# Optimization experiments

Hardware: AMD Instinct MI355X
Metric: run time of the kernel (lower is better)

Reference implementation:

```python
import jax, jax.numpy as jnp
import numpy as np

N, E, G = 10000, 160000, 64
F, C1, C2, C3, K, NC = 128, 128, 256, 512, 5, 10


def setup_inputs() -> dict:
    key = jax.random.key(0)
    ks = jax.random.split(key, 12)
    s = 0.05
    return {
        "x": jax.random.normal(ks[0], (N, F), dtype=jnp.float32),
        "edge_index": jax.random.randint(ks[1], (2, E), 0, N, dtype=jnp.int64),
        "batch": jnp.sort(jax.random.randint(ks[2], (N,), 0, G, dtype=jnp.int64)),
        "W_cheb": jax.random.normal(ks[3], (K, F, C1), dtype=jnp.float32) * s,
        "b_cheb": jnp.zeros((C1,), jnp.float32),
        "W_g1": jax.random.normal(ks[4], (C1, C2), dtype=jnp.float32) * s,
        "b_g1": jnp.zeros((C2,), jnp.float32),
        "W_g2": jax.random.normal(ks[5], (C2, C3), dtype=jnp.float32) * s,
        "b_g2": jnp.zeros((C3,), jnp.float32),
        "w_gate": jax.random.normal(ks[6], (C3, 1), dtype=jnp.float32) * s,
        "b_gate": jnp.zeros((1,), jnp.float32),
        "W_fc": jax.random.normal(ks[7], (C3, NC), dtype=jnp.float32) * s,
        "b_fc": jnp.zeros((NC,), jnp.float32),
    }


def _deg_inv_sqrt(deg):
    return jnp.where(deg > 0, jax.lax.rsqrt(jnp.maximum(deg, 1e-12)), 0.0)


def cheb_conv(x, src, dst, W, b):
    # PyG ChebConv, sym normalization, lambda_max=2 => scaled Laplacian = -D^-1/2 A D^-1/2
    ones = jnp.ones((src.shape[0],), x.dtype)
    deg = jax.ops.segment_sum(ones, src, num_segments=N)
    dinv = _deg_inv_sqrt(deg)
    w = -(dinv[src] * dinv[dst])  # [E]

    def prop(h):
        return jax.ops.segment_sum(w[:, None] * h[src], dst, num_segments=N)

    tx0 = x
    tx1 = prop(x)
    out = tx0 @ W[0] + tx1 @ W[1]
    for k in range(2, W.shape[0]):
        tx2 = 2.0 * prop(tx1) - tx0
        out = out + tx2 @ W[k]
        tx0, tx1 = tx1, tx2
    return out + b


def gcn_conv(x, src, dst, W, b):
    # PyG GCNConv: add self-loops, sym norm D~^-1/2 (A+I) D~^-1/2, transform then aggregate
    loop = jnp.arange(N, dtype=src.dtype)
    src_a = jnp.concatenate([src, loop])
    dst_a = jnp.concatenate([dst, loop])
    ones = jnp.ones((src_a.shape[0],), x.dtype)
    deg = jax.ops.segment_sum(ones, dst_a, num_segments=N)
    dinv = _deg_inv_sqrt(deg)
    norm = dinv[src_a] * dinv[dst_a]  # [E+N]
    h = x @ W
    return jax.ops.segment_sum(norm[:, None] * h[src_a], dst_a, num_segments=N) + b


def attention_pool(x, batch, w_gate, b_gate):
    logits = (x @ w_gate + b_gate)[:, 0]  # [N]
    m = jax.ops.segment_max(logits, batch, num_segments=G)
    e = jnp.exp(logits - m[batch])
    s = jax.ops.segment_sum(e, batch, num_segments=G)
    alpha = e / s[batch]
    return jax.ops.segment_sum(alpha[:, None] * x, batch, num_segments=G)  # [G, C3]


def reference(x, edge_index, batch, W_cheb, b_cheb, W_g1, b_g1, W_g2, b_g2,
              w_gate, b_gate, W_fc, b_fc):
    src, dst = edge_index[0], edge_index[1]
    h = jax.nn.relu(cheb_conv(x, src, dst, W_cheb, b_cheb))
    h = jax.nn.relu(gcn_conv(h, src, dst, W_g1, b_g1))
    h = jax.nn.relu(gcn_conv(h, src, dst, W_g2, b_g2))
    g = attention_pool(h, batch, w_gate, b_gate)
    logits = g @ W_fc + b_fc
    return jax.nn.log_softmax(logits, axis=1)
```

## Files before the change

kernel.cpp:

```cpp
#include <hip/hip_runtime.h>
#include <hip/hip_bf16.h>
#include <math.h>

#define N_NODES 10000
#define N_EDGES 160000
#define N_GRAPHS 64
#define F_IN    128
#define C1_DIM  128
#define C2_DIM  256
#define C3_DIM  512
#define K_CHEB  5
#define NCLS    10
#define TC      (K_CHEB * F_IN)

typedef short v8s __attribute__((ext_vector_type(8)));
typedef float v4f __attribute__((ext_vector_type(4)));

static __device__ __forceinline__ unsigned short f2bf(float f) {
    unsigned u = __float_as_uint(f);
    unsigned r = (u + 0x7FFFu + ((u >> 16) & 1u)) >> 16;
    return (unsigned short)r;
}
static __device__ __forceinline__ float bf_lo(unsigned u) { return __uint_as_float(u << 16); }
static __device__ __forceinline__ float bf_hi(unsigned u) { return __uint_as_float(u & 0xFFFF0000u); }

#define PREP_A (N_NODES * 32)
#define PREP_B (TC * C1_DIM)
#define PREP_C (C1_DIM * C2_DIM)
#define PREP_D (C2_DIM * C3_DIM)
#define PREP_E N_NODES
#define PREP_F N_NODES
#define PREP_G N_EDGES
#define PREP_TOTAL (PREP_A + PREP_B + PREP_C + PREP_D + PREP_E + PREP_F + PREP_G)
__global__ void prep_kernel(const float* __restrict__ x, unsigned short* __restrict__ tcat,
                            const float* __restrict__ Wcheb, unsigned short* __restrict__ Wcb_t,
                            const float* __restrict__ Wg1, unsigned short* __restrict__ Wg1_t,
                            const float* __restrict__ Wg2, unsigned short* __restrict__ Wg2_t,
                            const int* __restrict__ batch, int* __restrict__ gptr,
                            float* __restrict__ logits,
                            const int* __restrict__ src, const int* __restrict__ dst,
                            int* __restrict__ cnt_s, int* __restrict__ cnt_d) {
    int id = blockIdx.x * blockDim.x + threadIdx.x;
    if (id < PREP_A) {
        int n = id >> 5, f = (id & 31) * 4;
        float4 v = *(const float4*)(x + (size_t)n * F_IN + f);
        ushort4 o; o.x = f2bf(v.x); o.y = f2bf(v.y); o.z = f2bf(v.z); o.w = f2bf(v.w);
        *(ushort4*)(tcat + (size_t)n * TC + f) = o;
        return;
    }
    id -= PREP_A;
    if (id < PREP_B) {
        int k = id % TC, n = id / TC;
        Wcb_t[(size_t)n * TC + k] = f2bf(Wcheb[(size_t)k * C1_DIM + n]);
        return;
    }
    id -= PREP_B;
    if (id < PREP_C) {
        int k = id % C1_DIM, n = id / C1_DIM;
        Wg1_t[(size_t)n * C1_DIM + k] = f2bf(Wg1[(size_t)k * C2_DIM + n]);
        return;
    }
    id -= PREP_C;
    if (id < PREP_D) {
        int k = id % C2_DIM, n = id / C2_DIM;
        Wg2_t[(size_t)n * C2_DIM + k] = f2bf(Wg2[(size_t)k * C3_DIM + n]);
        return;
    }
    id -= PREP_D;
    if (id < PREP_E) {
        int i = id;
        int b = batch[i];
        if (i == 0) { for (int g = 0; g <= b; g++) gptr[g] = 0; }
        else {
            int bp = batch[i - 1];
            for (int g = bp + 1; g <= b; g++) gptr[g] = i;
        }
        if (i == N_NODES - 1) { for (int g = b + 1; g <= N_GRAPHS; g++) gptr[g] = N_NODES; }
        return;
    }
    id -= PREP_E;
    if (id < PREP_F) { logits[id] = 0.0f; return; }
    id -= PREP_F;
    if (id < PREP_G) {
        atomicAdd(&cnt_s[src[id]], 1);
        atomicAdd(&cnt_d[dst[id]], 1);
    }
}

__global__ __launch_bounds__(256) void fill_scan_kernel(
        const int* __restrict__ src, const int* __restrict__ dst,
        const int* __restrict__ cnt_s, const int* __restrict__ cnt_d,
        int* __restrict__ rowptr, int* __restrict__ fillc,
        int2* __restrict__ ecb, int2* __restrict__ egc, int E, int n) {
    __shared__ int ldsc[N_NODES];
    __shared__ int sums[256];
    int tid = threadIdx.x;
    for (int i = tid; i < n; i += 256) ldsc[i] = cnt_d[i];
    __syncthreads();
    int chunk = (n + 255) / 256;
    int s0 = min(n, tid * chunk), s1 = min(n, s0 + chunk);
    int loc = 0;
    for (int i = s0; i < s1; i++) loc += ldsc[i];
    sums[tid] = loc;
    __syncthreads();
    for (int off = 1; off < 256; off <<= 1) {
        int t = (tid >= off) ? sums[tid - off] : 0;
        __syncthreads();
        sums[tid] += t;
        __syncthreads();
    }
    int pre = sums[tid] - loc;
    for (int i = s0; i < s1; i++) { int v = ldsc[i]; ldsc[i] = pre; pre += v; }
    __syncthreads();
    if (blockIdx.x == 0) {
        for (int i = tid; i < n; i += 256) rowptr[i] = ldsc[i];
        if (tid == 255) rowptr[n] = pre;
    }
    int e = blockIdx.x * 256 + tid;
    if (e >= E) return;
    int s = src[e], d = dst[e];
    int pos = ldsc[d] + atomicAdd(&fillc[d], 1);
    int cs = cnt_s[s], cd = cnt_s[d];
    float ds = (cs > 0) ? rsqrtf((float)cs) : 0.0f;
    float dd = (cd > 0) ? rsqrtf((float)cd) : 0.0f;
    float nr = rsqrtf((float)cnt_d[s] + 1.0f) * rsqrtf((float)cnt_d[d] + 1.0f);
    ecb[pos] = make_int2(s, __float_as_int(-(ds * dd)));
    egc[pos] = make_int2(s, __float_as_int(nr));
}

__global__ __launch_bounds__(256) void gather_cheb_bf(
        const unsigned short* __restrict__ tb, const int* __restrict__ rowptr,
        const int2* __restrict__ edges,
        const unsigned short* __restrict__ base, float alpha, float beta,
        unsigned short* __restrict__ outc, int n) {
    int w = (blockIdx.x * blockDim.x + threadIdx.x) >> 6;
    int lane = threadIdx.x & 63;
    if (w >= n) return;
    w = __builtin_amdgcn_readfirstlane(w);
    int rs = __builtin_amdgcn_readfirstlane(rowptr[w]);
    int re = __builtin_amdgcn_readfirstlane(rowptr[w + 1]);
    float a0 = 0.0f, a1 = 0.0f;
    for (int b = rs; b < re; b += 64) {
        int nv = min(64, re - b);
        int cl = 0, wlb = 0;
        if (b + lane < re) { int2 e = edges[b + lane]; cl = e.x; wlb = e.y; }
        int nk = (nv + 15) & ~15;
        for (int j = 0; j < nk; j += 16) {
            int ss[16]; float ww[16]; unsigned uu[16];
            #pragma unroll
            for (int q = 0; q < 16; q++) {
                ss[q] = __builtin_amdgcn_readlane(cl, j + q);
                ww[q] = __uint_as_float((unsigned)__builtin_amdgcn_readlane(wlb, j + q));
            }
            #pragma unroll
            for (int q = 0; q < 16; q++)
                uu[q] = *(const unsigned*)(tb + (size_t)ss[q] * TC + lane * 2);
            #pragma unroll
            for (int q = 0; q < 16; q++) { a0 += ww[q] * bf_lo(uu[q]); a1 += ww[q] * bf_hi(uu[q]); }
        }
    }
    if (base) {
        unsigned ub = ((const unsigned*)(base + (size_t)w * TC))[lane];
        a0 = alpha * a0 + beta * bf_lo(ub);
        a1 = alpha * a1 + beta * bf_hi(ub);
    } else {
        a0 *= alpha; a1 *= alpha;
    }
    ushort2 o; o.x = f2bf(a0); o.y = f2bf(a1);
    *(ushort2*)(outc + (size_t)w * TC + lane * 2) = o;
}

template<int FPL>
__global__ __launch_bounds__(256) void gather_gcn_pre(
        const unsigned short* __restrict__ tb, const int* __restrict__ rowptr,
        const int2* __restrict__ edges,
        const int* __restrict__ cnt_d, unsigned short* __restrict__ z, int n) {
    const int C = FPL * 64;
    int w = (blockIdx.x * blockDim.x + threadIdx.x) >> 6;
    int lane = threadIdx.x & 63;
    if (w >= n) return;
    w = __builtin_amdgcn_readfirstlane(w);
    int rs = __builtin_amdgcn_readfirstlane(rowptr[w]);
    int re = __builtin_amdgcn_readfirstlane(rowptr[w + 1]);
    float acc[FPL];
    #pragma unroll
    for (int q = 0; q < FPL; q++) acc[q] = 0.0f;
    for (int b = rs; b < re; b += 64) {
        int nv = min(64, re - b);
        int cl = 0, wlb = 0;
        if (b + lane < re) { int2 e = edges[b + lane]; cl = e.x; wlb = e.y; }
        int nk = (nv + 15) & ~15;
        for (int j = 0; j < nk; j += 16) {
            int ss[16]; float ww[16];
            #pragma unroll
            for (int q = 0; q < 16; q++) {
                ss[q] = __builtin_amdgcn_readlane(cl, j + q);
                ww[q] = __uint_as_float((unsigned)__builtin_amdgcn_readlane(wlb, j + q));
            }
            if constexpr (FPL == 2) {
                unsigned uu[16];
                #pragma unroll
                for (int q = 0; q < 16; q++)
                    uu[q] = *(const unsigned*)(tb + (size_t)ss[q] * C + lane * 2);
                #pragma unroll
                for (int q = 0; q < 16; q++) { acc[0] += ww[q] * bf_lo(uu[q]); acc[1] += ww[q] * bf_hi(uu[q]); }
            } else {
                uint2 uu[16];
                #pragma unroll
                for (int q = 0; q < 16; q++)
                    uu[q] = *(const uint2*)(tb + (size_t)ss[q] * C + lane * 4);
                #pragma unroll
                for (int q = 0; q < 16; q++) {
                    acc[0] += ww[q] * bf_lo(uu[q].x); acc[1] += ww[q] * bf_hi(uu[q].x);
                    acc[2] += ww[q] * bf_lo(uu[q].y); acc[3] += ww[q] * bf_hi(uu[q].y);
                }
            }
        }
    }
    float sn = 1.0f / (float)(cnt_d[w] + 1);
    if constexpr (FPL == 2) {
        unsigned u = ((const unsigned*)(tb + (size_t)w * C))[lane];
        acc[0] += sn * bf_lo(u); acc[1] += sn * bf_hi(u);
        ushort2 o; o.x = f2bf(acc[0]); o.y = f2bf(acc[1]);
        *(ushort2*)(z + (size_t)w * C + lane * 2) = o;
    } else {
        uint2 u = ((const uint2*)(tb + (size_t)w * C))[lane];
        acc[0] += sn * bf_lo(u.x); acc[1] += sn * bf_hi(u.x);
        acc[2] += sn * bf_lo(u.y); acc[3] += sn * bf_hi(u.y);
        ushort4 o; o.x = f2bf(acc[0]); o.y = f2bf(acc[1]);
        o.z = f2bf(acc[2]); o.w = f2bf(acc[3]);
        *(ushort4*)(z + (size_t)w * C + lane * 4) = o;
    }
}

template<int JT, int KC>
__global__ __launch_bounds__(256) void gemm_bf16(
        const unsigned short* __restrict__ A, const unsigned short* __restrict__ Bt,
        const float* __restrict__ bias,
        unsigned short* __restrict__ Cb, const float* __restrict__ wg,
        float* __restrict__ logits, int M, int N) {
    int m0 = blockIdx.y * 64, n0 = blockIdx.x * (JT * 32);
    int wave = threadIdx.x >> 6, lane = threadIdx.x & 63;
    int wm = (wave & 1) * 32, wn = (wave >> 1) * (JT * 16);
    int l15 = lane & 15, quad = lane >> 4;

    v4f acc[2][JT];
    #pragma unroll
    for (int i = 0; i < 2; i++)
        #pragma unroll
        for (int j = 0; j < JT; j++) acc[i][j] = (v4f){0.f, 0.f, 0.f, 0.f};

    const unsigned short* Ab[2]; bool av[2];
    #pragma unroll
    for (int i = 0; i < 2; i++) {
        int row = m0 + wm + i * 16 + l15;
        av[i] = row < M;
        Ab[i] = A + (size_t)(av[i] ? row : 0) * KC + quad * 8;
    }
    const unsigned short* Bb[JT];
    #pragma unroll
    for (int j = 0; j < JT; j++) {
        int coln = n0 + wn + j * 16 + l15;
        Bb[j] = Bt + (size_t)coln * KC + quad * 8;
    }
    const v8s zero8 = {0, 0, 0, 0, 0, 0, 0, 0};

    #pragma unroll
    for (int k0 = 0; k0 < KC; k0 += 32) {
        v8s a[2], b[JT];
        #pragma unroll
        for (int i = 0; i < 2; i++) a[i] = av[i] ? *(const v8s*)(Ab[i] + k0) : zero8;
        #pragma unroll
        for (int j = 0; j < JT; j++) b[j] = *(const v8s*)(Bb[j] + k0);
        #pragma unroll
        for (int i = 0; i < 2; i++)
            #pragma unroll
            for (int j = 0; j < JT; j++)
                acc[i][j] = __builtin_amdgcn_mfma_f32_16x16x32_bf16(a[i], b[j], acc[i][j], 0, 0, 0);
    }

    float bv[JT], wgj[JT];
    #pragma unroll
    for (int j = 0; j < JT; j++) {
        int coln = n0 + wn + j * 16 + l15;
        bv[j] = bias[coln];
        wgj[j] = wg ? wg[coln] : 0.0f;
    }
    #pragma unroll
    for (int i = 0; i < 2; i++) {
        #pragma unroll
        for (int r = 0; r < 4; r++) {
            int row = m0 + wm + i * 16 + quad * 4 + r;
            if (row >= M) continue;
            float gval = 0.0f;
            #pragma unroll
            for (int j = 0; j < JT; j++) {
                int coln = n0 + wn + j * 16 + l15;
                float v = fmaxf(acc[i][j][r] + bv[j], 0.0f);
                Cb[(size_t)row * N + coln] = f2bf(v);
                gval += v * wgj[j];
            }
            if (wg) {
                #pragma unroll
                for (int off = 1; off < 16; off <<= 1) gval += __shfl_xor(gval, off);
                if (l15 == 0) atomicAdd(&logits[row], gval);
            }
        }
    }
}

__global__ __launch_bounds__(256) void pool_fc_kernel(
        const unsigned short* __restrict__ h3b,
        const float* __restrict__ logits, const int* __restrict__ gptr,
        const float* __restrict__ Wfc, const float* __restrict__ bfc,
        float* __restrict__ out) {
    __shared__ float red[256];
    __shared__ float pl[C3_DIM];
    int g = blockIdx.x, tid = threadIdx.x;
    int gs = gptr[g], ge = gptr[g + 1];
    float m = -INFINITY;
    for (int i = gs + tid; i < ge; i += 256) m = fmaxf(m, logits[i]);
    red[tid] = m; __syncthreads();
    for (int off = 128; off > 0; off >>= 1) {
        if (tid < off) red[tid] = fmaxf(red[tid], red[tid + off]);
        __syncthreads();
    }
    m = red[0]; __syncthreads();
    float s = 0.0f;
    for (int i = gs + tid; i < ge; i += 256) s += expf(logits[i] - m);
    red[tid] = s; __syncthreads();
    for (int off = 128; off > 0; off >>= 1) {
        if (tid < off) red[tid] += red[tid + off];
        __syncthreads();
    }
    s = red[0];
    float sinv = (s > 0.0f) ? 1.0f / s : 0.0f;
    float a0 = 0.0f, a1 = 0.0f;
    for (int i = gs; i < ge; i++) {
        float al = expf(logits[i] - m) * sinv;
        unsigned u = ((const unsigned*)(h3b + (size_t)i * C3_DIM))[tid];
        a0 += al * bf_lo(u);
        a1 += al * bf_hi(u);
    }
    pl[tid * 2 + 0] = a0;
    pl[tid * 2 + 1] = a1;
    __syncthreads();
    if (tid < 64) {
        float acc = -INFINITY;
        if (tid < NCLS) {
            acc = bfc[tid];
            for (int k = 0; k < C3_DIM; k++)
                acc += pl[k] * Wfc[k * NCLS + tid];
        }
        float mm = acc;
        #pragma unroll
        for (int off = 8; off > 0; off >>= 1) mm = fmaxf(mm, __shfl_xor(mm, off, 16));
        float e = (tid < NCLS) ? expf(acc - mm) : 0.0f;
        float ss = e;
        #pragma unroll
        for (int off = 8; off > 0; off >>= 1) ss += __shfl_xor(ss, off, 16);
        if (tid < NCLS) out[g * NCLS + tid] = acc - mm - logf(ss);
    }
}

extern "C" void kernel_launch(void* const* d_in, const int* in_sizes, int n_in,
                              void* d_out, int out_size, void* d_ws, size_t ws_size,
                              hipStream_t stream) {
    const float* x      = (const float*)d_in[0];
    const int*   ei     = (const int*)d_in[1];
    const int*   batch  = (const int*)d_in[2];
    const float* W_cheb = (const float*)d_in[3];
    const float* b_cheb = (const float*)d_in[4];
    const float* W_g1   = (const float*)d_in[5];
    const float* b_g1   = (const float*)d_in[6];
    const float* W_g2   = (const float*)d_in[7];
    const float* b_g2   = (const float*)d_in[8];
    const float* w_gate = (const float*)d_in[9];
    const float* W_fc   = (const float*)d_in[11];
    const float* b_fc   = (const float*)d_in[12];
    const int* src = ei;
    const int* dst = ei + N_EDGES;
    float* out = (float*)d_out;

    const int N = N_NODES, E = N_EDGES, G = N_GRAPHS;

    char* Wp = (char*)d_ws;
    auto alloc = [&](size_t bytes) {
        void* p = Wp;
        Wp += (bytes + 255) & ~(size_t)255;
        return p;
    };
    int*   cnt3    = (int*)alloc((size_t)3 * N * 4);
    int*   cnt_s   = cnt3;
    int*   cnt_d   = cnt3 + N;
    int*   fillc   = cnt3 + 2 * N;
    int*   rowptr  = (int*)alloc((N + 1) * 4);
    int2*  ecb     = (int2*)alloc((size_t)E * 8);
    int2*  egc     = (int2*)alloc((size_t)E * 8);
    unsigned short* tcat  = (unsigned short*)alloc((size_t)N * TC * 2);
    unsigned short* h1b   = (unsigned short*)alloc((size_t)N * C1_DIM * 2);
    unsigned short* z1b   = (unsigned short*)alloc((size_t)N * C1_DIM * 2);
    unsigned short* h2b   = (unsigned short*)alloc((size_t)N * C2_DIM * 2);
    unsigned short* z2b   = (unsigned short*)alloc((size_t)N * C2_DIM * 2);
    unsigned short* h3b   = (unsigned short*)alloc((size_t)N * C3_DIM * 2);
    unsigned short* Wcb_t = (unsigned short*)alloc((size_t)TC * C1_DIM * 2);
    unsigned short* Wg1_t = (unsigned short*)alloc((size_t)C1_DIM * C2_DIM * 2);
    unsigned short* Wg2_t = (unsigned short*)alloc((size_t)C2_DIM * C3_DIM * 2);
    float* logits  = (float*)alloc(N * 4);
    int*   gptr    = (int*)alloc((G + 1) * 4);

    dim3 blk(256);
    auto cdiv = [](int a, int b) { return (a + b - 1) / b; };

    hipMemsetAsync(cnt3, 0, (size_t)3 * N * sizeof(int), stream);
    hipLaunchKernelGGL(prep_kernel, dim3(cdiv(PREP_TOTAL, 256)), blk, 0, stream,
                       x, tcat, W_cheb, Wcb_t, W_g1, Wg1_t, W_g2, Wg2_t,
                       batch, gptr, logits, src, dst, cnt_s, cnt_d);

    hipLaunchKernelGGL(fill_scan_kernel, dim3(cdiv(E, 256)), blk, 0, stream,
                       src, dst, cnt_s, cnt_d, rowptr, fillc, ecb, egc, E, N);

    const int NWB = cdiv(N, 4);

    hipLaunchKernelGGL(gather_cheb_bf, dim3(NWB), blk, 0, stream,
                       tcat + 0 * F_IN, rowptr, ecb,
                       (const unsigned short*)nullptr, 1.0f, 0.0f, tcat + 1 * F_IN, N);
    hipLaunchKernelGGL(gather_cheb_bf, dim3(NWB), blk, 0, stream,
                       tcat + 1 * F_IN, rowptr, ecb,
                       tcat + 0 * F_IN, 2.0f, -1.0f, tcat + 2 * F_IN, N);
    hipLaunchKernelGGL(gather_cheb_bf, dim3(NWB), blk, 0, stream,
                       tcat + 2 * F_IN, rowptr, ecb,
                       tcat + 1 * F_IN, 2.0f, -1.0f, tcat + 3 * F_IN, N);
    hipLaunchKernelGGL(gather_cheb_bf, dim3(NWB), blk, 0, stream,
                       tcat + 3 * F_IN, rowptr, ecb,
                       tcat + 2 * F_IN, 2.0f, -1.0f, tcat + 4 * F_IN, N);

    hipLaunchKernelGGL((gemm_bf16<2, TC>), dim3(C1_DIM / 64, cdiv(N, 64)), blk, 0, stream,
                       tcat, Wcb_t, b_cheb, h1b,
                       (const float*)nullptr, (float*)nullptr, N, C1_DIM);

    hipLaunchKernelGGL(gather_gcn_pre<2>, dim3(NWB), blk, 0, stream,
                       h1b, rowptr, egc, cnt_d, z1b, N);
    hipLaunchKernelGGL((gemm_bf16<4, C1_DIM>), dim3(C2_DIM / 128, cdiv(N, 64)), blk, 0, stream,
                       z1b, Wg1_t, b_g1, h2b,
                       (const float*)nullptr, (float*)nullptr, N, C2_DIM);

    hipLaunchKernelGGL(gather_gcn_pre<4>, dim3(NWB), blk, 0, stream,
                       h2b, rowptr, egc, cnt_d, z2b, N);
    hipLaunchKernelGGL((gemm_bf16<4, C2_DIM>), dim3(C3_DIM / 128, cdiv(N, 64)), blk, 0, stream,
                       z2b, Wg2_t, b_g2, h3b,
                       w_gate, logits, N, C3_DIM);

    hipLaunchKernelGGL(pool_fc_kernel, dim3(G), blk, 0, stream,
                       h3b, logits, gptr, W_fc, b_fc, out);
}
```

Before: 290.5 us.

## Fuse GCN gather into GEMM via LDS tile and split attention pooling across blocks

Each GCN layer's neighbor aggregation is now computed straight into a swizzled LDS tile inside the GEMM kernel, which removes the separate gather kernels and the z1/z2 intermediate buffers and their global round trips. The aggregation is recomputed once per column block: twice for layer 1 and twice for layer 2, which uses a wider JT=8 tile. Pooling is split into 8 node slices per graph that accumulate with float atomics, and the last block to finish does the FC and log-softmax. The cost is redundant gather work, larger LDS use that may lower occupancy, and non-deterministic atomic summation order.

```diff
diff --git a/kernel.cpp b/kernel.cpp
--- a/kernel.cpp
+++ b/kernel.cpp
@@ -30,14 +30,15 @@
 #define PREP_D (C2_DIM * C3_DIM)
 #define PREP_E N_NODES
 #define PREP_F N_NODES
+#define PREP_H (N_GRAPHS * C3_DIM)
 #define PREP_G N_EDGES
-#define PREP_TOTAL (PREP_A + PREP_B + PREP_C + PREP_D + PREP_E + PREP_F + PREP_G)
+#define PREP_TOTAL (PREP_A + PREP_B + PREP_C + PREP_D + PREP_E + PREP_F + PREP_H + PREP_G)
 __global__ void prep_kernel(const float* __restrict__ x, unsigned short* __restrict__ tcat,
                             const float* __restrict__ Wcheb, unsigned short* __restrict__ Wcb_t,
                             const float* __restrict__ Wg1, unsigned short* __restrict__ Wg1_t,
                             const float* __restrict__ Wg2, unsigned short* __restrict__ Wg2_t,
                             const int* __restrict__ batch, int* __restrict__ gptr,
-                            float* __restrict__ logits,
+                            float* __restrict__ logits, float* __restrict__ pooled,
                             const int* __restrict__ src, const int* __restrict__ dst,
                             int* __restrict__ cnt_s, int* __restrict__ cnt_d) {
     int id = blockIdx.x * blockDim.x + threadIdx.x;
@@ -81,6 +82,8 @@
     id -= PREP_E;
     if (id < PREP_F) { logits[id] = 0.0f; return; }
     id -= PREP_F;
+    if (id < PREP_H) { pooled[id] = 0.0f; return; }
+    id -= PREP_H;
     if (id < PREP_G) {
         atomicAdd(&cnt_s[src[id]], 1);
         atomicAdd(&cnt_d[dst[id]], 1);
@@ -170,75 +173,11 @@
     *(ushort2*)(outc + (size_t)w * TC + lane * 2) = o;
 }
 
-template<int FPL>
-__global__ __launch_bounds__(256) void gather_gcn_pre(
-        const unsigned short* __restrict__ tb, const int* __restrict__ rowptr,
-        const int2* __restrict__ edges,
-        const int* __restrict__ cnt_d, unsigned short* __restrict__ z, int n) {
-    const int C = FPL * 64;
-    int w = (blockIdx.x * blockDim.x + threadIdx.x) >> 6;
-    int lane = threadIdx.x & 63;
-    if (w >= n) return;
-    w = __builtin_amdgcn_readfirstlane(w);
-    int rs = __builtin_amdgcn_readfirstlane(rowptr[w]);
-    int re = __builtin_amdgcn_readfirstlane(rowptr[w + 1]);
-    float acc[FPL];
-    #pragma unroll
-    for (int q = 0; q < FPL; q++) acc[q] = 0.0f;
-    for (int b = rs; b < re; b += 64) {
-        int nv = min(64, re - b);
-        int cl = 0, wlb = 0;
-        if (b + lane < re) { int2 e = edges[b + lane]; cl = e.x; wlb = e.y; }
-        int nk = (nv + 15) & ~15;
-        for (int j = 0; j < nk; j += 16) {
-            int ss[16]; float ww[16];
-            #pragma unroll
-            for (int q = 0; q < 16; q++) {
-                ss[q] = __builtin_amdgcn_readlane(cl, j + q);
-                ww[q] = __uint_as_float((unsigned)__builtin_amdgcn_readlane(wlb, j + q));
-            }
-            if constexpr (FPL == 2) {
-                unsigned uu[16];
-                #pragma unroll
-                for (int q = 0; q < 16; q++)
-                    uu[q] = *(const unsigned*)(tb + (size_t)ss[q] * C + lane * 2);
-                #pragma unroll
-                for (int q = 0; q < 16; q++) { acc[0] += ww[q] * bf_lo(uu[q]); acc[1] += ww[q] * bf_hi(uu[q]); }
-            } else {
-                uint2 uu[16];
-                #pragma unroll
-                for (int q = 0; q < 16; q++)
-                    uu[q] = *(const uint2*)(tb + (size_t)ss[q] * C + lane * 4);
-                #pragma unroll
-                for (int q = 0; q < 16; q++) {
-                    acc[0] += ww[q] * bf_lo(uu[q].x); acc[1] += ww[q] * bf_hi(uu[q].x);
-                    acc[2] += ww[q] * bf_lo(uu[q].y); acc[3] += ww[q] * bf_hi(uu[q].y);
-                }
-            }
-        }
-    }
-    float sn = 1.0f / (float)(cnt_d[w] + 1);
-    if constexpr (FPL == 2) {
-        unsigned u = ((const unsigned*)(tb + (size_t)w * C))[lane];
-        acc[0] += sn * bf_lo(u); acc[1] += sn * bf_hi(u);
-        ushort2 o; o.x = f2bf(acc[0]); o.y = f2bf(acc[1]);
-        *(ushort2*)(z + (size_t)w * C + lane * 2) = o;
-    } else {
-        uint2 u = ((const uint2*)(tb + (size_t)w * C))[lane];
-        acc[0] += sn * bf_lo(u.x); acc[1] += sn * bf_hi(u.x);
-        acc[2] += sn * bf_lo(u.y); acc[3] += sn * bf_hi(u.y);
-        ushort4 o; o.x = f2bf(acc[0]); o.y = f2bf(acc[1]);
-        o.z = f2bf(acc[2]); o.w = f2bf(acc[3]);
-        *(ushort4*)(z + (size_t)w * C + lane * 4) = o;
-    }
-}
-
 template<int JT, int KC>
 __global__ __launch_bounds__(256) void gemm_bf16(
         const unsigned short* __restrict__ A, const unsigned short* __restrict__ Bt,
         const float* __restrict__ bias,
-        unsigned short* __restrict__ Cb, const float* __restrict__ wg,
-        float* __restrict__ logits, int M, int N) {
+        unsigned short* __restrict__ Cb, int M, int N) {
     int m0 = blockIdx.y * 64, n0 = blockIdx.x * (JT * 32);
     int wave = threadIdx.x >> 6, lane = threadIdx.x & 63;
     int wm = (wave & 1) * 32, wn = (wave >> 1) * (JT * 16);
@@ -279,6 +218,135 @@
                 acc[i][j] = __builtin_amdgcn_mfma_f32_16x16x32_bf16(a[i], b[j], acc[i][j], 0, 0, 0);
     }
 
+    float bv[JT];
+    #pragma unroll
+    for (int j = 0; j < JT; j++) bv[j] = bias[n0 + wn + j * 16 + l15];
+    #pragma unroll
+    for (int i = 0; i < 2; i++) {
+        #pragma unroll
+        for (int r = 0; r < 4; r++) {
+            int row = m0 + wm + i * 16 + quad * 4 + r;
+            if (row >= M) continue;
+            #pragma unroll
+            for (int j = 0; j < JT; j++) {
+                int coln = n0 + wn + j * 16 + l15;
+                float v = fmaxf(acc[i][j][r] + bv[j], 0.0f);
+                Cb[(size_t)row * N + coln] = f2bf(v);
+            }
+        }
+    }
+}
+
+template<int JT, int KC>
+__global__ __launch_bounds__(256) void gemm_gcn_fused(
+        const unsigned short* __restrict__ h_in,
+        const int* __restrict__ rowptr, const int2* __restrict__ edges,
+        const int* __restrict__ cnt_d,
+        const unsigned short* __restrict__ Bt, const float* __restrict__ bias,
+        unsigned short* __restrict__ Cb, const float* __restrict__ wg,
+        float* __restrict__ logits, int M, int N) {
+    constexpr int FPL = KC / 64;
+    __shared__ unsigned short zt[64 * KC];
+    int m0 = blockIdx.y * 64, n0 = blockIdx.x * (JT * 32);
+    int wave = threadIdx.x >> 6, lane = threadIdx.x & 63;
+
+    for (int r = 0; r < 16; ++r) {
+        int wl = wave * 16 + r;
+        int w  = m0 + wl;
+        float acc[FPL];
+        #pragma unroll
+        for (int q = 0; q < FPL; q++) acc[q] = 0.0f;
+        if (w < M) {
+            int rs = __builtin_amdgcn_readfirstlane(rowptr[w]);
+            int re = __builtin_amdgcn_readfirstlane(rowptr[w + 1]);
+            for (int b = rs; b < re; b += 64) {
+                int cl = 0, wlb = 0;
+                if (b + lane < re) { int2 e = edges[b + lane]; cl = e.x; wlb = e.y; }
+                int nk = (min(64, re - b) + 15) & ~15;
+                for (int j = 0; j < nk; j += 16) {
+                    int ss[16]; float ww[16];
+                    #pragma unroll
+                    for (int q = 0; q < 16; q++) {
+                        ss[q] = __builtin_amdgcn_readlane(cl, j + q);
+                        ww[q] = __uint_as_float((unsigned)__builtin_amdgcn_readlane(wlb, j + q));
+                    }
+                    if constexpr (FPL == 2) {
+                        unsigned uu[16];
+                        #pragma unroll
+                        for (int q = 0; q < 16; q++)
+                            uu[q] = *(const unsigned*)(h_in + (size_t)ss[q] * KC + lane * 2);
+                        #pragma unroll
+                        for (int q = 0; q < 16; q++) { acc[0] += ww[q] * bf_lo(uu[q]); acc[1] += ww[q] * bf_hi(uu[q]); }
+                    } else {
+                        uint2 uu[16];
+                        #pragma unroll
+                        for (int q = 0; q < 16; q++)
+                            uu[q] = *(const uint2*)(h_in + (size_t)ss[q] * KC + lane * 4);
+                        #pragma unroll
+                        for (int q = 0; q < 16; q++) {
+                            acc[0] += ww[q] * bf_lo(uu[q].x); acc[1] += ww[q] * bf_hi(uu[q].x);
+                            acc[2] += ww[q] * bf_lo(uu[q].y); acc[3] += ww[q] * bf_hi(uu[q].y);
+                        }
+                    }
+                }
+            }
+            float sn = 1.0f / (float)(cnt_d[w] + 1);
+            if constexpr (FPL == 2) {
+                unsigned u = *(const unsigned*)(h_in + (size_t)w * KC + lane * 2);
+                acc[0] += sn * bf_lo(u); acc[1] += sn * bf_hi(u);
+            } else {
+                uint2 u = *(const uint2*)(h_in + (size_t)w * KC + lane * 4);
+                acc[0] += sn * bf_lo(u.x); acc[1] += sn * bf_hi(u.x);
+                acc[2] += sn * bf_lo(u.y); acc[3] += sn * bf_hi(u.y);
+            }
+        }
+        if constexpr (FPL == 2) {
+            ushort2 o; o.x = f2bf(acc[0]); o.y = f2bf(acc[1]);
+            unsigned col = (lane * 4u) ^ ((unsigned)(wl & 7) << 4);
+            *(ushort2*)((char*)zt + (size_t)wl * (KC * 2) + col) = o;
+        } else {
+            ushort4 o; o.x = f2bf(acc[0]); o.y = f2bf(acc[1]);
+            o.z = f2bf(acc[2]); o.w = f2bf(acc[3]);
+            unsigned col = (lane * 8u) ^ ((unsigned)(wl & 7) << 4);
+            *(ushort4*)((char*)zt + (size_t)wl * (KC * 2) + col) = o;
+        }
+    }
+    __syncthreads();
+
+    int wm = (wave & 1) * 32, wn = (wave >> 1) * (JT * 16);
+    int l15 = lane & 15, quad = lane >> 4;
+
+    v4f acc2[2][JT];
+    #pragma unroll
+    for (int i = 0; i < 2; i++)
+        #pragma unroll
+        for (int j = 0; j < JT; j++) acc2[i][j] = (v4f){0.f, 0.f, 0.f, 0.f};
+
+    const unsigned short* Bb[JT];
+    #pragma unroll
+    for (int j = 0; j < JT; j++) {
+        int coln = n0 + wn + j * 16 + l15;
+        Bb[j] = Bt + (size_t)coln * KC + quad * 8;
+    }
+
+    #pragma unroll
+    for (int k0 = 0; k0 < KC; k0 += 32) {
+        v8s a[2], b[JT];
+        #pragma unroll
+        for (int i = 0; i < 2; i++) {
+            int rowl = wm + i * 16 + l15;
+            unsigned col = ((unsigned)(k0 * 2 + quad * 16)) ^ ((unsigned)(rowl & 7) << 4);
+            a[i] = *(const v8s*)((const char*)zt + (size_t)rowl * (KC * 2) + col);
+        }
+        #pragma unroll
+        for (int j = 0; j < JT; j++) b[j] = *(const v8s*)(Bb[j] + k0);
+        #pragma unroll
+        for (int i = 0; i < 2; i++)
+            #pragma unroll
+            for (int j = 0; j < JT; j++)
+                acc2[i][j] = __builtin_amdgcn_mfma_f32_16x16x32_bf16(a[i], b[j], acc2[i][j], 0, 0, 0);
+    }
+
     float bv[JT], wgj[JT];
     #pragma unroll
     for (int j = 0; j < JT; j++) {
@@ -296,7 +364,7 @@
             #pragma unroll
             for (int j = 0; j < JT; j++) {
                 int coln = n0 + wn + j * 16 + l15;
-                float v = fmaxf(acc[i][j][r] + bv[j], 0.0f);
+                float v = fmaxf(acc2[i][j][r] + bv[j], 0.0f);
                 Cb[(size_t)row * N + coln] = f2bf(v);
                 gval += v * wgj[j];
             }
@@ -312,11 +380,13 @@
 __global__ __launch_bounds__(256) void pool_fc_kernel(
         const unsigned short* __restrict__ h3b,
         const float* __restrict__ logits, const int* __restrict__ gptr,
+        float* __restrict__ pooled, int* __restrict__ pcnt,
         const float* __restrict__ Wfc, const float* __restrict__ bfc,
         float* __restrict__ out) {
     __shared__ float red[256];
     __shared__ float pl[C3_DIM];
-    int g = blockIdx.x, tid = threadIdx.x;
+    __shared__ int lastf;
+    int g = blockIdx.x, sl = blockIdx.y, tid = threadIdx.x;
     int gs = gptr[g], ge = gptr[g + 1];
     float m = -INFINITY;
     for (int i = gs + tid; i < ge; i += 256) m = fmaxf(m, logits[i]);
@@ -335,31 +405,50 @@
     }
     s = red[0];
     float sinv = (s > 0.0f) ? 1.0f / s : 0.0f;
+    int cnt = ge - gs;
+    int i0 = gs + (cnt * sl) / 8;
+    int i1 = gs + (cnt * (sl + 1)) / 8;
     float a0 = 0.0f, a1 = 0.0f;
-    for (int i = gs; i < ge; i++) {
+    for (int i = i0; i < i1; i++) {
         float al = expf(logits[i] - m) * sinv;
         unsigned u = ((const unsigned*)(h3b + (size_t)i * C3_DIM))[tid];
         a0 += al * bf_lo(u);
         a1 += al * bf_hi(u);
     }
-    pl[tid * 2 + 0] = a0;
-    pl[tid * 2 + 1] = a1;
+    if (i1 > i0) {
+        atomicAdd(&pooled[(size_t)g * C3_DIM + tid * 2 + 0], a0);
+        atomicAdd(&pooled[(size_t)g * C3_DIM + tid * 2 + 1], a1);
+    }
     __syncthreads();
-    if (tid < 64) {
-        float acc = -INFINITY;
-        if (tid < NCLS) {
-            acc = bfc[tid];
-            for (int k = 0; k < C3_DIM; k++)
-                acc += pl[k] * Wfc[k * NCLS + tid];
-        }
-        float mm = acc;
-        #pragma unroll
-        for (int off = 8; off > 0; off >>= 1) mm = fmaxf(mm, __shfl_xor(mm, off, 16));
-        float e = (tid < NCLS) ? expf(acc - mm) : 0.0f;
-        float ss = e;
-        #pragma unroll
-        for (int off = 8; off > 0; off >>= 1) ss += __shfl_xor(ss, off, 16);
-        if (tid < NCLS) out[g * NCLS + tid] = acc - mm - logf(ss);
+    if (tid == 0) {
+        __threadfence();
+        int old = atomicAdd(&pcnt[g], 1);
+        lastf = (old == 7) ? 1 : 0;
+    }
+    __syncthreads();
+    if (lastf) {
+        __threadfence();
+        pl[tid * 2 + 0] = __hip_atomic_load(&pooled[(size_t)g * C3_DIM + tid * 2 + 0],
+                                            __ATOMIC_RELAXED, __HIP_MEMORY_SCOPE_AGENT);
+        pl[tid * 2 + 1] = __hip_atomic_load(&pooled[(size_t)g * C3_DIM + tid * 2 + 1],
+                                            __ATOMIC_RELAXED, __HIP_MEMORY_SCOPE_AGENT);
+        __syncthreads();
+        if (tid < 64) {
+            float acc = -INFINITY;
+            if (tid < NCLS) {
+                acc = bfc[tid];
+                for (int k = 0; k < C3_DIM; k++)
+                    acc += pl[k] * Wfc[k * NCLS + tid];
+            }
+            float mm = acc;
+            #pragma unroll
+            for (int off = 8; off > 0; off >>= 1) mm = fmaxf(mm, __shfl_xor(mm, off, 16));
+            float e = (tid < NCLS) ? expf(acc - mm) : 0.0f;
+            float ss = e;
+            #pragma unroll
+            for (int off = 8; off > 0; off >>= 1) ss += __shfl_xor(ss, off, 16);
+            if (tid < NCLS) out[g * NCLS + tid] = acc - mm - logf(ss);
+        }
     }
 }
 
@@ -390,32 +479,32 @@
         Wp += (bytes + 255) & ~(size_t)255;
         return p;
     };
-    int*   cnt3    = (int*)alloc((size_t)3 * N * 4);
+    int*   cnt3    = (int*)alloc(((size_t)3 * N + G) * 4);
     int*   cnt_s   = cnt3;
     int*   cnt_d   = cnt3 + N;
     int*   fillc   = cnt3 + 2 * N;
+    int*   pcnt    = cnt3 + 3 * N;
     int*   rowptr  = (int*)alloc((N + 1) * 4);
     int2*  ecb     = (int2*)alloc((size_t)E * 8);
     int2*  egc     = (int2*)alloc((size_t)E * 8);
     unsigned short* tcat  = (unsigned short*)alloc((size_t)N * TC * 2);
     unsigned short* h1b   = (unsigned short*)alloc((size_t)N * C1_DIM * 2);
-    unsigned short* z1b   = (unsigned short*)alloc((size_t)N * C1_DIM * 2);
     unsigned short* h2b   = (unsigned short*)alloc((size_t)N * C2_DIM * 2);
-    unsigned short* z2b   = (unsigned short*)alloc((size_t)N * C2_DIM * 2);
     unsigned short* h3b   = (unsigned short*)alloc((size_t)N * C3_DIM * 2);
     unsigned short* Wcb_t = (unsigned short*)alloc((size_t)TC * C1_DIM * 2);
     unsigned short* Wg1_t = (unsigned short*)alloc((size_t)C1_DIM * C2_DIM * 2);
     unsigned short* Wg2_t = (unsigned short*)alloc((size_t)C2_DIM * C3_DIM * 2);
     float* logits  = (float*)alloc(N * 4);
     int*   gptr    = (int*)alloc((G + 1) * 4);
+    float* pooled  = (float*)alloc((size_t)G * C3_DIM * 4);
 
     dim3 blk(256);
     auto cdiv = [](int a, int b) { return (a + b - 1) / b; };
 
-    hipMemsetAsync(cnt3, 0, (size_t)3 * N * sizeof(int), stream);
+    hipMemsetAsync(cnt3, 0, ((size_t)3 * N + G) * sizeof(int), stream);
     hipLaunchKernelGGL(prep_kernel, dim3(cdiv(PREP_TOTAL, 256)), blk, 0, stream,
                        x, tcat, W_cheb, Wcb_t, W_g1, Wg1_t, W_g2, Wg2_t,
-                       batch, gptr, logits, src, dst, cnt_s, cnt_d);
+                       batch, gptr, logits, pooled, src, dst, cnt_s, cnt_d);
 
     hipLaunchKernelGGL(fill_scan_kernel, dim3(cdiv(E, 256)), blk, 0, stream,
                        src, dst, cnt_s, cnt_d, rowptr, fillc, ecb, egc, E, N);
@@ -436,21 +525,16 @@
                        tcat + 2 * F_IN, 2.0f, -1.0f, tcat + 4 * F_IN, N);
 
     hipLaunchKernelGGL((gemm_bf16<2, TC>), dim3(C1_DIM / 64, cdiv(N, 64)), blk, 0, stream,
-                       tcat, Wcb_t, b_cheb, h1b,
-                       (const float*)nullptr, (float*)nullptr, N, C1_DIM);
-
-    hipLaunchKernelGGL(gather_gcn_pre<2>, dim3(NWB), blk, 0, stream,
-                       h1b, rowptr, egc, cnt_d, z1b, N);
-    hipLaunchKernelGGL((gemm_bf16<4, C1_DIM>), dim3(C2_DIM / 128, cdiv(N, 64)), blk, 0, stream,
-                       z1b, Wg1_t, b_g1, h2b,
+                       tcat, Wcb_t, b_cheb, h1b, N, C1_DIM);
+
+    hipLaunchKernelGGL((gemm_gcn_fused<4, C1_DIM>), dim3(C2_DIM / 128, cdiv(N, 64)), blk, 0, stream,
+                       h1b, rowptr, egc, cnt_d, Wg1_t, b_g1, h2b,
                        (const float*)nullptr, (float*)nullptr, N, C2_DIM);
 
-    hipLaunchKernelGGL(gather_gcn_pre<4>, dim3(NWB), blk, 0, stream,
-                       h2b, rowptr, egc, cnt_d, z2b, N);
-    hipLaunchKernelGGL((gemm_bf16<4, C2_DIM>), dim3(C3_DIM / 128, cdiv(N, 64)), blk, 0, stream,
-                       z2b, Wg2_t, b_g2, h3b,
+    hipLaunchKernelGGL((gemm_gcn_fused<8, C2_DIM>), dim3(C3_DIM / 256, cdiv(N, 64)), blk, 0, stream,
+                       h2b, rowptr, egc, cnt_d, Wg2_t, b_g2, h3b,
                        w_gate, logits, N, C3_DIM);
 
-    hipLaunchKernelGGL(pool_fc_kernel, dim3(G), blk, 0, stream,
-                       h3b, logits, gptr, W_fc, b_fc, out);
-}
+    hipLaunchKernelGGL(pool_fc_kernel, dim3(G, 8), blk, 0, stream,
+                       h3b, logits, gptr, pooled, pcnt, W_fc, b_fc, out);
+}
```

Measured after the change: 319.7 us. 10.1% more time.

## Split attention pooling across 8 blocks per graph with atomic reduction

Applied to the files above, without the earlier changes.

The pool kernel now launches 8 slices per graph. Each slice accumulates the softmax-weighted sum over a contiguous node range and atomically adds it into a zeroed global pooled buffer. A per-graph counter picks the last-finishing block, which then does the FC layer and log-softmax. The aim is to raise parallelism beyond 64 blocks in the serial pooling loop, at the cost of each slice redoing the max and sum reductions, float atomics, and a threadfence handshake.

```diff
diff --git a/kernel.cpp b/kernel.cpp
--- a/kernel.cpp
+++ b/kernel.cpp
@@ -24,20 +24,22 @@
 static __device__ __forceinline__ float bf_lo(unsigned u) { return __uint_as_float(u << 16); }
 static __device__ __forceinline__ float bf_hi(unsigned u) { return __uint_as_float(u & 0xFFFF0000u); }
 
+
 #define PREP_A (N_NODES * 32)
 #define PREP_B (TC * C1_DIM)
 #define PREP_C (C1_DIM * C2_DIM)
 #define PREP_D (C2_DIM * C3_DIM)
 #define PREP_E N_NODES
 #define PREP_F N_NODES
+#define PREP_H (N_GRAPHS * C3_DIM)
 #define PREP_G N_EDGES
-#define PREP_TOTAL (PREP_A + PREP_B + PREP_C + PREP_D + PREP_E + PREP_F + PREP_G)
+#define PREP_TOTAL (PREP_A + PREP_B + PREP_C + PREP_D + PREP_E + PREP_F + PREP_H + PREP_G)
 __global__ void prep_kernel(const float* __restrict__ x, unsigned short* __restrict__ tcat,
                             const float* __restrict__ Wcheb, unsigned short* __restrict__ Wcb_t,
                             const float* __restrict__ Wg1, unsigned short* __restrict__ Wg1_t,
                             const float* __restrict__ Wg2, unsigned short* __restrict__ Wg2_t,
                             const int* __restrict__ batch, int* __restrict__ gptr,
-                            float* __restrict__ logits,
+                            float* __restrict__ logits, float* __restrict__ pooled,
                             const int* __restrict__ src, const int* __restrict__ dst,
                             int* __restrict__ cnt_s, int* __restrict__ cnt_d) {
     int id = blockIdx.x * blockDim.x + threadIdx.x;
@@ -81,6 +83,8 @@
     id -= PREP_E;
     if (id < PREP_F) { logits[id] = 0.0f; return; }
     id -= PREP_F;
+    if (id < PREP_H) { pooled[id] = 0.0f; return; }
+    id -= PREP_H;
     if (id < PREP_G) {
         atomicAdd(&cnt_s[src[id]], 1);
         atomicAdd(&cnt_d[dst[id]], 1);
@@ -312,11 +316,13 @@
 __global__ __launch_bounds__(256) void pool_fc_kernel(
         const unsigned short* __restrict__ h3b,
         const float* __restrict__ logits, const int* __restrict__ gptr,
+        float* __restrict__ pooled, int* __restrict__ pcnt,
         const float* __restrict__ Wfc, const float* __restrict__ bfc,
         float* __restrict__ out) {
     __shared__ float red[256];
     __shared__ float pl[C3_DIM];
-    int g = blockIdx.x, tid = threadIdx.x;
+    __shared__ int lastf;
+    int g = blockIdx.x, sl = blockIdx.y, tid = threadIdx.x;
     int gs = gptr[g], ge = gptr[g + 1];
     float m = -INFINITY;
     for (int i = gs + tid; i < ge; i += 256) m = fmaxf(m, logits[i]);
@@ -335,31 +341,50 @@
     }
     s = red[0];
     float sinv = (s > 0.0f) ? 1.0f / s : 0.0f;
+    int cnt = ge - gs;
+    int i0 = gs + (cnt * sl) / 8;
+    int i1 = gs + (cnt * (sl + 1)) / 8;
     float a0 = 0.0f, a1 = 0.0f;
-    for (int i = gs; i < ge; i++) {
+    for (int i = i0; i < i1; i++) {
         float al = expf(logits[i] - m) * sinv;
         unsigned u = ((const unsigned*)(h3b + (size_t)i * C3_DIM))[tid];
         a0 += al * bf_lo(u);
         a1 += al * bf_hi(u);
     }
-    pl[tid * 2 + 0] = a0;
-    pl[tid * 2 + 1] = a1;
+    if (i1 > i0) {
+        atomicAdd(&pooled[(size_t)g * C3_DIM + tid * 2 + 0], a0);
+        atomicAdd(&pooled[(size_t)g * C3_DIM + tid * 2 + 1], a1);
+    }
     __syncthreads();
-    if (tid < 64) {
-        float acc = -INFINITY;
-        if (tid < NCLS) {
-            acc = bfc[tid];
-            for (int k = 0; k < C3_DIM; k++)
-                acc += pl[k] * Wfc[k * NCLS + tid];
+    if (tid == 0) {
+        __threadfence();
+        int old = atomicAdd(&pcnt[g], 1);
+        lastf = (old == 7) ? 1 : 0;
+    }
+    __syncthreads();
+    if (lastf) {
+        __threadfence();
+        pl[tid * 2 + 0] = __hip_atomic_load(&pooled[(size_t)g * C3_DIM + tid * 2 + 0],
+                                            __ATOMIC_RELAXED, __HIP_MEMORY_SCOPE_AGENT);
+        pl[tid * 2 + 1] = __hip_atomic_load(&pooled[(size_t)g * C3_DIM + tid * 2 + 1],
+                                            __ATOMIC_RELAXED, __HIP_MEMORY_SCOPE_AGENT);
+        __syncthreads();
+        if (tid < 64) {
+            float acc = -INFINITY;
+            if (tid < NCLS) {
+                acc = bfc[tid];
+                for (int k = 0; k < C3_DIM; k++)
+                    acc += pl[k] * Wfc[k * NCLS + tid];
+            }
+            float mm = acc;
+            #pragma unroll
+            for (int off = 8; off > 0; off >>= 1) mm = fmaxf(mm, __shfl_xor(mm, off, 16));
+            float e = (tid < NCLS) ? expf(acc - mm) : 0.0f;
+            float ss = e;
+            #pragma unroll
+            for (int off = 8; off > 0; off >>= 1) ss += __shfl_xor(ss, off, 16);
+            if (tid < NCLS) out[g * NCLS + tid] = acc - mm - logf(ss);
         }
-        float mm = acc;
-        #pragma unroll
-        for (int off = 8; off > 0; off >>= 1) mm = fmaxf(mm, __shfl_xor(mm, off, 16));
-        float e = (tid < NCLS) ? expf(acc - mm) : 0.0f;
-        float ss = e;
-        #pragma unroll
-        for (int off = 8; off > 0; off >>= 1) ss += __shfl_xor(ss, off, 16);
-        if (tid < NCLS) out[g * NCLS + tid] = acc - mm - logf(ss);
     }
 }
 
@@ -390,10 +415,11 @@
         Wp += (bytes + 255) & ~(size_t)255;
         return p;
     };
-    int*   cnt3    = (int*)alloc((size_t)3 * N * 4);
+    int*   cnt3    = (int*)alloc(((size_t)3 * N + G) * 4);
     int*   cnt_s   = cnt3;
     int*   cnt_d   = cnt3 + N;
     int*   fillc   = cnt3 + 2 * N;
+    int*   pcnt    = cnt3 + 3 * N;
     int*   rowptr  = (int*)alloc((N + 1) * 4);
     int2*  ecb     = (int2*)alloc((size_t)E * 8);
     int2*  egc     = (int2*)alloc((size_t)E * 8);
@@ -408,14 +434,15 @@
     unsigned short* Wg2_t = (unsigned short*)alloc((size_t)C2_DIM * C3_DIM * 2);
     float* logits  = (float*)alloc(N * 4);
     int*   gptr    = (int*)alloc((G + 1) * 4);
+    float* pooled  = (float*)alloc((size_t)G * C3_DIM * 4);
 
     dim3 blk(256);
     auto cdiv = [](int a, int b) { return (a + b - 1) / b; };
 
-    hipMemsetAsync(cnt3, 0, (size_t)3 * N * sizeof(int), stream);
+    hipMemsetAsync(cnt3, 0, ((size_t)3 * N + G) * sizeof(int), stream);
     hipLaunchKernelGGL(prep_kernel, dim3(cdiv(PREP_TOTAL, 256)), blk, 0, stream,
                        x, tcat, W_cheb, Wcb_t, W_g1, Wg1_t, W_g2, Wg2_t,
-                       batch, gptr, logits, src, dst, cnt_s, cnt_d);
+                       batch, gptr, logits, pooled, src, dst, cnt_s, cnt_d);
 
     hipLaunchKernelGGL(fill_scan_kernel, dim3(cdiv(E, 256)), blk, 0, stream,
                        src, dst, cnt_s, cnt_d, rowptr, fillc, ecb, egc, E, N);
@@ -451,6 +478,6 @@
                        z2b, Wg2_t, b_g2, h3b,
                        w_gate, logits, N, C3_DIM);
 
-    hipLaunchKernelGGL(pool_fc_kernel, dim3(G), blk, 0, stream,
-                       h3b, logits, gptr, W_fc, b_fc, out);
-}
+    hipLaunchKernelGGL(pool_fc_kernel, dim3(G, 8), blk, 0, stream,
+                       h3b, logits, gptr, pooled, pcnt, W_fc, b_fc, out);
+}
```

New measurement: 267.6 us. 1.09x faster.
